# Performance work log

Measured on AMD Instinct MI355X. Metric: run time of the kernel, lower is better.

Reference implementation:

```python
import jax, jax.numpy as jnp
import numpy as np
import math

PAD_IDX = 1
BOS_IDX = 2
B, S, T = 32, 128, 64
E, H, L, V = 256, 512, 2, 32000


def _lstm_cell(gates, c):
    # torch gate order: i, f, g, o
    i, f, g, o = jnp.split(gates, 4, axis=-1)
    c_new = jax.nn.sigmoid(f) * c + jax.nn.sigmoid(i) * jnp.tanh(g)
    h_new = jax.nn.sigmoid(o) * jnp.tanh(c_new)
    return h_new, c_new


def _run_lstm_layer(x_tbi, Wih, Whh, b, h0, c0):
    def step(carry, x_t):
        h, c = carry
        h2, c2 = _lstm_cell(x_t @ Wih + h @ Whh + b, c)
        return (h2, c2), h2
    (hT, cT), ys = jax.lax.scan(step, (h0, c0), x_tbi)
    return ys, hT, cT


def setup_inputs() -> dict:
    key = jax.random.key(0)
    ks = iter(jax.random.split(key, 40))
    def w(shape, s=0.05):
        return jax.random.normal(next(ks), shape, jnp.float32) * s
    inp = {
        'src_tokens': jax.random.randint(next(ks), (B, S), 0, V, dtype=jnp.int32),
        'tgt_tokens': jax.random.randint(next(ks), (B, T), 0, V, dtype=jnp.int32),
        'src_emb': w((V, E), 0.02),
        'tgt_emb': w((V, E), 0.02),
        'enc_Wih0': w((E, 4 * H)), 'enc_Whh0': w((H, 4 * H)), 'enc_b0': jnp.zeros((4 * H,), jnp.float32),
        'enc_Wih1': w((H, 4 * H)), 'enc_Whh1': w((H, 4 * H)), 'enc_b1': jnp.zeros((4 * H,), jnp.float32),
        'dec_Wih0': w((E + H, 4 * H)), 'dec_Whh0': w((H, 4 * H)), 'dec_b0': jnp.zeros((4 * H,), jnp.float32),
        'dec_Wih1': w((H, 4 * H)), 'dec_Whh1': w((H, 4 * H)), 'dec_b1': jnp.zeros((4 * H,), jnp.float32),
        'attn_W': w((2 * H, H)), 'attn_b': jnp.zeros((H,), jnp.float32),
        'v_w': w((H,)),
        'coal_w': w((L, 1), 0.5), 'coal_b': jnp.zeros((1,), jnp.float32),
        'out_W': w((2 * H + E, V)), 'out_b': jnp.zeros((V,), jnp.float32),
    }
    return inp


def reference(src_tokens, tgt_tokens, src_emb, tgt_emb,
              enc_Wih0, enc_Whh0, enc_b0, enc_Wih1, enc_Whh1, enc_b1,
              dec_Wih0, dec_Whh0, dec_b0, dec_Wih1, dec_Whh1, dec_b1,
              attn_W, attn_b, v_w, coal_w, coal_b, out_W, out_b):
    Bq = src_tokens.shape[0]
    sqrtE_src = np.float32(math.sqrt(src_emb.shape[1]))
    sqrtE_tgt = np.float32(math.sqrt(tgt_emb.shape[1]))

    # ---- Encoder (2-layer LSTM, batch_first; dropout=0 eval) ----
    x = (src_emb[src_tokens] * sqrtE_src).transpose(1, 0, 2)  # (S,B,E)
    z = jnp.zeros((Bq, H), jnp.float32)
    ys0, hA, cA = _run_lstm_layer(x, enc_Wih0, enc_Whh0, enc_b0, z, z)
    ys1, hB, cB = _run_lstm_layer(ys0, enc_Wih1, enc_Whh1, enc_b1, z, z)
    enc_out = ys1.transpose(1, 0, 2)          # (B,S,H)
    hidden = jnp.stack([hA, hB])              # (L,B,H)
    cell = jnp.stack([cA, cB])

    mask = src_tokens != PAD_IDX              # (B,S)
    Wq, We = attn_W[:H], attn_W[H:]
    enc_proj = enc_out @ We                   # (B,S,H) loop-invariant part of attn linear

    def dec_step(carry, tok):
        h, c = carry                          # (L,B,H) each
        emb = jax.nn.relu(tgt_emb[tok] * sqrtE_tgt)          # (B,E)
        # faithful raw reshape (L,B,H) -> (B,H,L), coalesce layers
        q = jax.nn.relu(h.reshape(Bq, H, L) @ coal_w + coal_b)[..., 0]  # (B,H)
        e = jnp.tanh(enc_proj + (q @ Wq + attn_b)[:, None, :])          # (B,S,H)
        score = e @ v_w                                                 # (B,S)
        score = jnp.where(mask, score, np.float32(-1e10))
        a = jax.nn.softmax(score, axis=1)
        wctx = jnp.einsum('bs,bsh->bh', a, enc_out)                     # (B,H)
        xin = jnp.concatenate([emb, wctx], axis=-1)                     # (B,E+H)
        h0n, c0n = _lstm_cell(xin @ dec_Wih0 + h[0] @ dec_Whh0 + dec_b0, c[0])
        h1n, c1n = _lstm_cell(h0n @ dec_Wih1 + h[1] @ dec_Whh1 + dec_b1, c[1])
        logits = jnp.concatenate([h1n, wctx, emb], axis=-1) @ out_W + out_b  # (B,V)
        return (jnp.stack([h0n, h1n]), jnp.stack([c0n, c1n])), logits

    (hF, cF), outs = jax.lax.scan(dec_step, (hidden, cell), tgt_tokens[:, :-1].T)
    first = jnp.full((Bq, 1, out_b.shape[0]), np.float32(BOS_IDX))  # decoder_outputs[:,0]=BOS_IDX
    dec_outputs = jnp.concatenate([first, outs.transpose(1, 0, 2)], axis=1)  # (B,T,V)
    return dec_outputs, hF, cF
```

## Files before the change

kernel.cpp:

```cpp
#include <hip/hip_runtime.h>
#include <hip/hip_bf16.h>

typedef __bf16 bf16x8 __attribute__((ext_vector_type(8)));
typedef float f32x4 __attribute__((ext_vector_type(4)));
typedef unsigned long long u64;

#define DEV static __device__ __forceinline__

constexpr int Bq = 32, Sq = 128, Tq = 64, Eq = 256, Hq = 512, Vq = 32000;
constexpr int TD = 63;
constexpr int KOUT = 1280;
constexpr float SQRTE = 16.0f;

DEV float sigf(float x) { return 1.0f / (1.0f + __expf(-x)); }
DEV float tanh_fast(float x) {
    float ax = fabsf(x);
    float t = __expf(-2.f * ax);
    float r = (1.f - t) / (1.f + t);
    return x < 0.f ? -r : r;
}
DEV float tanh_c(float x) {
    float xc = fminf(fmaxf(x, -15.f), 15.f);
    float t = __expf(2.f * xc);
    return (t - 1.f) / (t + 1.f);
}

DEV u64 ldc(const u64* p) {
    return __hip_atomic_load(p, __ATOMIC_RELAXED, __HIP_MEMORY_SCOPE_AGENT);
}
DEV unsigned ldc32(const unsigned* p) {
    return __hip_atomic_load(p, __ATOMIC_RELAXED, __HIP_MEMORY_SCOPE_AGENT);
}
DEV void stc(u64* p, u64 v) {
    __hip_atomic_store(p, v, __ATOMIC_RELAXED, __HIP_MEMORY_SCOPE_AGENT);
}
DEV void stc32(unsigned* p, unsigned v) {
    __hip_atomic_store(p, v, __ATOMIC_RELAXED, __HIP_MEMORY_SCOPE_AGENT);
}
DEV unsigned short bfbits(float f) {
    __bf16 h = (__bf16)f;
    return __builtin_bit_cast(unsigned short, h);
}
DEV float bf2f(unsigned short u) {
    __bf16 h = __builtin_bit_cast(__bf16, u);
    return (float)h;
}
DEV u64 pack4bf(float a, float b, float c, float d) {
    return (u64)bfbits(a) | ((u64)bfbits(b) << 16) |
           ((u64)bfbits(c) << 32) | ((u64)bfbits(d) << 48);
}
DEV u64 pack2f(float a, float b) {
    return (u64)__float_as_uint(a) | ((u64)__float_as_uint(b) << 32);
}
template<bool C> DEV u64 ld64g(const u64* p) { return C ? ldc(p) : *p; }
template<bool C> DEV void st64g(u64* p, u64 v) { if (C) stc(p, v); else *p = v; }
DEV void drain_vm() { asm volatile("s_waitcnt vmcnt(0)" ::: "memory"); }

DEV void encwait(unsigned* flags, unsigned need0, unsigned need1) {
    __syncthreads();
    if (threadIdx.x < 64) {
        int lane = threadIdx.x;
        unsigned need = (lane < 32) ? need0 : need1;
        for (;;) {
            unsigned v = ldc32(flags + lane * 32);
            if (__all((int)(v >= need))) break;
            __builtin_amdgcn_s_sleep(1);
        }
    }
    __syncthreads();
}

__global__ __launch_bounds__(256) void k_embed_src(const int* __restrict__ tok,
                                                   const float* __restrict__ emb,
                                                   __hip_bfloat16* __restrict__ x)
{
    int idx = blockIdx.x * 256 + threadIdx.x;
    int e = idx & (Eq - 1);
    int r = idx >> 8;
    int b = r & 31, t = r >> 5;
    x[idx] = __float2bfloat16(emb[(size_t)tok[b * Sq + t] * Eq + e] * SQRTE);
}

__global__ __launch_bounds__(256) void k_embed_tgt(const int* __restrict__ tok,
                                                   const float* __restrict__ emb,
                                                   __hip_bfloat16* __restrict__ embt,
                                                   __hip_bfloat16* __restrict__ Xout)
{
    int idx = blockIdx.x * 256 + threadIdx.x;
    int e = idx & (Eq - 1);
    int r = idx >> 8;
    int b = r & 31, t = r >> 5;
    float v = fmaxf(0.f, emb[(size_t)tok[b * Tq + t] * Eq + e] * SQRTE);
    embt[idx] = __float2bfloat16(v);
    Xout[(size_t)r * KOUT + 1024 + e] = __float2bfloat16(v);
}

__global__ __launch_bounds__(256) void k_transpose_bf16(const float* __restrict__ W,
                                                        __hip_bfloat16* __restrict__ Wt,
                                                        int K, int N)
{
    __shared__ float tile[32][33];
    int nb = blockIdx.x * 32, kb = blockIdx.y * 32;
    int c = threadIdx.x & 31, r4 = threadIdx.x >> 5;
    for (int i = 0; i < 32; i += 8)
        tile[r4 + i][c] = W[(size_t)(kb + r4 + i) * N + nb + c];
    __syncthreads();
    for (int i = 0; i < 32; i += 8) {
        int rr = r4 + i;
        Wt[(size_t)(nb + rr) * K + kb + c] = __float2bfloat16(tile[c][rr]);
    }
}

struct TD10 {
    const float* s[10];
    __hip_bfloat16* d[10];
    int K[10];
    int N[10];
};
__global__ __launch_bounds__(256) void k_transpose_multi(TD10 td)
{
    __shared__ float tile[32][33];
    int m = blockIdx.y;
    int K = td.K[m], N = td.N[m];
    int ntn = N >> 5;
    int nb = (blockIdx.x % ntn) * 32;
    int kb = (blockIdx.x / ntn) * 32;
    if (kb >= K) return;
    const float* W = td.s[m];
    __hip_bfloat16* Wt = td.d[m];
    int c = threadIdx.x & 31, r4 = threadIdx.x >> 5;
    for (int i = 0; i < 32; i += 8)
        tile[r4 + i][c] = W[(size_t)(kb + r4 + i) * N + nb + c];
    __syncthreads();
    for (int i = 0; i < 32; i += 8) {
        int rr = r4 + i;
        Wt[(size_t)(nb + rr) * K + kb + c] = __float2bfloat16(tile[c][rr]);
    }
}

template<bool C>
DEV void stage_a(const u64* src, __bf16* As) {
    int tx = threadIdx.x;
#pragma unroll
    for (int p = 0; p < 8; ++p) {
        int c = tx + p * 256;
        int row = c >> 6, kc = c & 63;
        u64 v0 = ld64g<C>(src + c * 2);
        u64 v1 = ld64g<C>(src + c * 2 + 1);
        int kd = kc ^ (row & 7);
        *(u64*)(As + row * 512 + kd * 8) = v0;
        *(u64*)(As + row * 512 + kd * 8 + 4) = v1;
    }
}

DEV void mfma_pass(const __bf16* As, const unsigned short* BT, int colB,
                   int kg, int fr, f32x4* acc) {
    const unsigned short* bp = BT + (size_t)colB * 512 + kg * 8;
    int f7 = fr & 7;
#pragma unroll
    for (int k0 = 0; k0 < 512; k0 += 32) {
        int cidx = ((k0 >> 3) | kg) ^ f7;
        bf16x8 bfv = *(const bf16x8*)(bp + k0);
        bf16x8 af0 = *(const bf16x8*)(As + fr * 512 + cidx * 8);
        bf16x8 af1 = *(const bf16x8*)(As + (16 + fr) * 512 + cidx * 8);
        acc[0] = __builtin_amdgcn_mfma_f32_16x16x32_bf16(af0, bfv, acc[0], 0, 0, 0);
        acc[1] = __builtin_amdgcn_mfma_f32_16x16x32_bf16(af1, bfv, acc[1], 0, 0, 0);
    }
}

DEV void mfma_gates(const __bf16* As0, const __bf16* As1,
                    const __hip_bfloat16* B0T, const __hip_bfloat16* B1T,
                    int j0, float* gbuf)
{
    int tx = threadIdx.x, w = tx >> 6, lane = tx & 63;
    int fr = lane & 15, kg = lane >> 4;
    int colB = w * 512 + j0 + fr;
    f32x4 acc[2];
    acc[0] = (f32x4){0.f, 0.f, 0.f, 0.f};
    acc[1] = (f32x4){0.f, 0.f, 0.f, 0.f};
    mfma_pass(As0, (const unsigned short*)B0T, colB, kg, fr, acc);
    if (B1T) mfma_pass(As1, (const unsigned short*)B1T, colB, kg, fr, acc);
    __syncthreads();
    float* gw = gbuf + w * 512;
#pragma unroll
    for (int m = 0; m < 2; ++m)
#pragma unroll
        for (int qd = 0; qd < 4; ++qd)
            gw[(m * 16 + kg * 4 + qd) * 16 + fr] = acc[m][qd];
    __syncthreads();
}

template<bool C>
DEV void cell_epi(const float* gbuf,
                  const __hip_bfloat16* xpart, const float* bias,
                  float* cbuf, u64* hb, u64* hf,
                  __hip_bfloat16* eb, int ebs, int j0)
{
    int tx = threadIdx.x;
    if (tx >= 128) return;
    int b = tx >> 2, jg = tx & 3;
    int jj0 = jg * 4;
    int j = j0 + jj0;
    float g[4][4];
#pragma unroll
    for (int gi = 0; gi < 4; ++gi) {
        int idx = gi * 512 + b * 16 + jj0;
        float4 gv = *(const float4*)(gbuf + idx);
        g[gi][0] = gv.x; g[gi][1] = gv.y; g[gi][2] = gv.z; g[gi][3] = gv.w;
        if (xpart) {
            u64 xv = *(const u64*)((const unsigned short*)xpart + b * 2048 + gi * 512 + j);
#pragma unroll
            for (int e = 0; e < 4; ++e)
                g[gi][e] += bf2f((unsigned short)(xv >> (16 * e)));
        }
        if (bias) {
            float4 bv = *(const float4*)(bias + gi * 512 + j);
            g[gi][0] += bv.x; g[gi][1] += bv.y; g[gi][2] += bv.z; g[gi][3] += bv.w;
        }
    }
    float4 cv = *(float4*)(cbuf + b * 512 + j);
    float cc[4] = {cv.x, cv.y, cv.z, cv.w};
    float hv[4];
#pragma unroll
    for (int e = 0; e < 4; ++e) {
        float cn = sigf(g[1][e]) * cc[e] + sigf(g[0][e]) * tanh_fast(g[2][e]);
        cc[e] = cn;
        hv[e] = sigf(g[3][e]) * tanh_fast(cn);
    }
    *(float4*)(cbuf + b * 512 + j) = make_float4(cc[0], cc[1], cc[2], cc[3]);
    u64 hpk = pack4bf(hv[0], hv[1], hv[2], hv[3]);
    st64g<C>(hb + ((b * 512 + j) >> 2), hpk);
    st64g<C>(hf + ((b * 512 + j) >> 1), pack2f(hv[0], hv[1]));
    st64g<C>(hf + ((b * 512 + j) >> 1) + 1, pack2f(hv[2], hv[3]));
    if (eb) st64g<C>((u64*)(eb + (size_t)b * ebs + j), hpk);
}

__global__ __launch_bounds__(256) void k_enc_persist(
    const __hip_bfloat16* __restrict__ X0b,
    const __hip_bfloat16* __restrict__ eWhh0T, const __hip_bfloat16* __restrict__ eWih1T,
    const __hip_bfloat16* __restrict__ eWhh1T, const float* __restrict__ eb1,
    __hip_bfloat16* __restrict__ h0b, __hip_bfloat16* __restrict__ h1b,
    float* __restrict__ h0f, float* __restrict__ h1f,
    float* __restrict__ c0, float* __restrict__ c1,
    __hip_bfloat16* __restrict__ ys0b,
    __hip_bfloat16* __restrict__ encb,
    unsigned* __restrict__ flags)
{
    __shared__ __align__(16) char shm[65536];
    __bf16* As0 = (__bf16*)shm;
    __bf16* As1 = (__bf16*)(shm + 32768);
    bool lay1 = blockIdx.x >= 32;
    int j0 = (blockIdx.x & 31) * 16;

    if (!lay1) {
        for (int t = 0; t < 128; ++t) {
            encwait(flags, (unsigned)t, 0u);
            stage_a<true>((const u64*)(h0b + (t & 1) * 16384), As0);
            __syncthreads();
            mfma_gates(As0, nullptr, eWhh0T, nullptr, j0, (float*)As0);
            cell_epi<true>((float*)As0, X0b + (size_t)t * 32 * 2048, nullptr,
                           c0, (u64*)(h0b + ((t + 1) & 1) * 16384), (u64*)h0f,
                           ys0b + (size_t)t * 16384, 512, j0);
            __syncthreads();
            if (threadIdx.x == 0) {
                drain_vm();
                stc32(flags + blockIdx.x * 32, (unsigned)(t + 1));
            }
        }
    } else {
        for (int s = 0; s < 128; ++s) {
            encwait(flags, (unsigned)(s + 1), (unsigned)s);
            stage_a<true>((const u64*)(ys0b + (size_t)s * 16384), As0);
            stage_a<true>((const u64*)(h1b + (s & 1) * 16384), As1);
            __syncthreads();
            mfma_gates(As0, As1, eWih1T, eWhh1T, j0, (float*)As0);
            cell_epi<true>((float*)As0, nullptr, eb1,
                           c1, (u64*)(h1b + ((s + 1) & 1) * 16384), (u64*)h1f,
                           encb + s * 512, 128 * 512, j0);
            __syncthreads();
            if (threadIdx.x == 0) {
                drain_vm();
                stc32(flags + blockIdx.x * 32, (unsigned)(s + 1));
            }
        }
    }
}

__global__ __launch_bounds__(256) void k_dattn2(
    const __hip_bfloat16* __restrict__ enc_projb, const __hip_bfloat16* __restrict__ enc_outb,
    const int* __restrict__ src_tok, const float* __restrict__ v_w,
    const float* __restrict__ attn_W, const float* __restrict__ attn_b,
    const float* __restrict__ coal_w, const float* __restrict__ coal_b,
    const float* __restrict__ h0fc, const float* __restrict__ h1fc,
    __hip_bfloat16* __restrict__ wctxb, __hip_bfloat16* __restrict__ XoutT)
{
    __shared__ float q[512];
    __shared__ float aqs[512];
    __shared__ float vws[512];
    __shared__ float ws[128];
    __shared__ float rinvs;
    int b = blockIdx.x, tx = threadIdx.x;

    const float* hrow = (b < 16) ? (h0fc + b * 1024) : (h1fc + (b - 16) * 1024);
    float cw0 = coal_w[0], cw1 = coal_w[1], cb = coal_b[0];
    for (int j = tx; j < 512; j += 256) {
        float2 pv = *(const float2*)(hrow + 2 * j);
        q[j] = fmaxf(0.f, pv.x * cw0 + pv.y * cw1 + cb);
    }
    for (int i = tx; i < 512; i += 256) vws[i] = v_w[i];
    __syncthreads();
    float a0 = attn_b[tx], a1 = attn_b[tx + 256];
#pragma unroll 8
    for (int j = 0; j < 512; ++j) {
        float qj = q[j];
        a0 += qj * attn_W[(size_t)j * 512 + tx];
        a1 += qj * attn_W[(size_t)j * 512 + tx + 256];
    }
    aqs[tx] = a0; aqs[tx + 256] = a1;
    __syncthreads();
    int s = tx >> 1, half = tx & 1;
    const unsigned short* epr = (const unsigned short*)enc_projb
                                + ((size_t)(b * 128 + s)) * 512 + half * 256;
    float s0 = 0.f, s1 = 0.f, s2 = 0.f, s3 = 0.f;
#pragma unroll 4
    for (int ii = 0; ii < 256; ii += 8) {
        bf16x8 f8 = *(const bf16x8*)(epr + ii);
        int ib = half * 256 + ii;
        s0 += tanh_c((float)f8[0] + aqs[ib])     * vws[ib];
        s1 += tanh_c((float)f8[1] + aqs[ib + 1]) * vws[ib + 1];
        s2 += tanh_c((float)f8[2] + aqs[ib + 2]) * vws[ib + 2];
        s3 += tanh_c((float)f8[3] + aqs[ib + 3]) * vws[ib + 3];
        s0 += tanh_c((float)f8[4] + aqs[ib + 4]) * vws[ib + 4];
        s1 += tanh_c((float)f8[5] + aqs[ib + 5]) * vws[ib + 5];
        s2 += tanh_c((float)f8[6] + aqs[ib + 6]) * vws[ib + 6];
        s3 += tanh_c((float)f8[7] + aqs[ib + 7]) * vws[ib + 7];
    }
    float p = (s0 + s1) + (s2 + s3);
    p += __shfl_xor(p, 1, 64);
    if (half == 0)
        ws[s] = (src_tok[b * 128 + s] != 1) ? __expf(p) : 0.f;
    __syncthreads();
    if (tx < 64) {
        float ss = ws[tx] + ws[tx + 64];
#pragma unroll
        for (int o = 32; o > 0; o >>= 1) ss += __shfl_down(ss, o, 64);
        if (tx == 0) rinvs = 1.0f / ss;
    }
    __syncthreads();
    float rinv = rinvs;
    const unsigned short* eo = (const unsigned short*)enc_outb + (size_t)b * 65536;
    int i0 = tx * 2;
    float c0a = 0.f, c1a = 0.f;
#pragma unroll 4
    for (int s2i = 0; s2i < 128; ++s2i) {
        unsigned pk2 = *(const unsigned*)(eo + (size_t)s2i * 512 + i0);
        float wv = ws[s2i];
        c0a += wv * bf2f((unsigned short)(pk2 & 0xffffu));
        c1a += wv * bf2f((unsigned short)(pk2 >> 16));
    }
    c0a *= rinv; c1a *= rinv;
    unsigned pk = (unsigned)bfbits(c0a) | ((unsigned)bfbits(c1a) << 16);
    *((unsigned*)wctxb + ((b * 512 + i0) >> 1)) = pk;
    *((unsigned*)XoutT + (((size_t)b * KOUT + 512 + i0) >> 1)) = pk;
}

__global__ __launch_bounds__(256) void k_rec(
    const __hip_bfloat16* __restrict__ A0, const __hip_bfloat16* __restrict__ B0T,
    const __hip_bfloat16* __restrict__ A1, const __hip_bfloat16* __restrict__ B1T,
    const __hip_bfloat16* __restrict__ xpart, const float* __restrict__ bias,
    float* __restrict__ cbuf, float* __restrict__ hf, __hip_bfloat16* __restrict__ hb,
    __hip_bfloat16* __restrict__ ebf16, int ebs)
{
    __shared__ __align__(16) char shm[65536];
    __bf16* As0 = (__bf16*)shm;
    __bf16* As1 = (__bf16*)(shm + 32768);
    int j0 = blockIdx.x * 16;
    stage_a<false>((const u64*)A0, As0);
    stage_a<false>((const u64*)A1, As1);
    __syncthreads();
    mfma_gates(As0, As1, B0T, B1T, j0, (float*)As0);
    cell_epi<false>((float*)As0, xpart, bias, cbuf, (u64*)hb, (u64*)hf, ebf16, ebs, j0);
}

__global__ __launch_bounds__(256) void k_mfma(
    const __hip_bfloat16* __restrict__ A, const __hip_bfloat16* __restrict__ BT,
    const float* __restrict__ bias, float* __restrict__ Cf,
    __hip_bfloat16* __restrict__ Cb, int M, int N, int K)
{
    __shared__ __bf16 As[128][72];
    __shared__ __bf16 Bs[128][72];
    const unsigned short* Aw = (const unsigned short*)A;
    const unsigned short* Bw = (const unsigned short*)BT;
    int n0 = blockIdx.x * 128, m0 = blockIdx.y * 128;
    int tx = threadIdx.x;
    int w = tx >> 6, lane = tx & 63;
    int wm = (w >> 1) * 64, wn = (w & 1) * 64;
    int fr = lane & 15, kg = lane >> 4;
    f32x4 acc[4][4];
#pragma unroll
    for (int mi = 0; mi < 4; mi++)
#pragma unroll
        for (int ni = 0; ni < 4; ni++) acc[mi][ni] = (f32x4){0.f, 0.f, 0.f, 0.f};

    for (int k0 = 0; k0 < K; k0 += 64) {
        __syncthreads();
#pragma unroll
        for (int p = 0; p < 4; p++) {
            int ch = tx + p * 256;
            int r = ch >> 3, cc = (ch & 7) * 8;
            uint4 va = {0u, 0u, 0u, 0u};
            int m = m0 + r;
            if (m < M) va = *(const uint4*)(Aw + (size_t)m * K + k0 + cc);
            *(uint4*)(&As[r][cc]) = va;
            uint4 vb = *(const uint4*)(Bw + (size_t)(n0 + r) * K + k0 + cc);
            *(uint4*)(&Bs[r][cc]) = vb;
        }
        __syncthreads();
#pragma unroll
        for (int kk = 0; kk < 64; kk += 32) {
            bf16x8 af[4], bfv[4];
#pragma unroll
            for (int i = 0; i < 4; i++) {
                af[i]  = *(const bf16x8*)(&As[wm + i * 16 + fr][kk + kg * 8]);
                bfv[i] = *(const bf16x8*)(&Bs[wn + i * 16 + fr][kk + kg * 8]);
            }
#pragma unroll
            for (int mi = 0; mi < 4; mi++)
#pragma unroll
                for (int ni = 0; ni < 4; ni++)
                    acc[mi][ni] = __builtin_amdgcn_mfma_f32_16x16x32_bf16(
                        af[mi], bfv[ni], acc[mi][ni], 0, 0, 0);
        }
    }
#pragma unroll
    for (int ni = 0; ni < 4; ni++) {
        int n = n0 + wn + ni * 16 + fr;
        float bv = bias ? bias[n] : 0.f;
#pragma unroll
        for (int mi = 0; mi < 4; mi++) {
#pragma unroll
            for (int qd = 0; qd < 4; qd++) {
                int R = m0 + wm + mi * 16 + kg * 4 + qd;
                if (R < M) {
                    float v = acc[mi][ni][qd] + bv;
                    if (Cf) Cf[(size_t)R * N + n] = v;
                    else    Cb[(size_t)R * N + n] = __float2bfloat16(v);
                }
            }
        }
    }
}

__global__ __launch_bounds__(256) void k_init_dec(
    const float* __restrict__ h0e, const float* __restrict__ h1e,
    const float* __restrict__ c0e, const float* __restrict__ c1e,
    float* __restrict__ h0fd, float* __restrict__ h1fd,
    __hip_bfloat16* __restrict__ h0bd, __hip_bfloat16* __restrict__ h1bd,
    float* __restrict__ c0d, float* __restrict__ c1d)
{
    int idx = blockIdx.x * 256 + threadIdx.x;
    float a = h0e[idx], b = h1e[idx];
    h0fd[idx] = a; h1fd[idx] = b;
    h0bd[idx] = __float2bfloat16(a);
    h1bd[idx] = __float2bfloat16(b);
    c0d[idx] = c0e[idx];
    c1d[idx] = c1e[idx];
}

__global__ __launch_bounds__(256) void k_bos(float* __restrict__ out)
{
    int b = blockIdx.y;
    int i = blockIdx.x * 256 + threadIdx.x;
    out[(size_t)b * (Tq * Vq) + i] = 2.0f;
}

__global__ __launch_bounds__(256) void k_finalize(
    const float* __restrict__ h0f, const float* __restrict__ h1f,
    const float* __restrict__ c0f, const float* __restrict__ c1f,
    float* __restrict__ out)
{
    int idx = blockIdx.x * 256 + threadIdx.x;
    size_t base = (size_t)Bq * Tq * Vq;
    out[base + idx] = h0f[idx];
    out[base + 16384 + idx] = h1f[idx];
    out[base + 32768 + idx] = c0f[idx];
    out[base + 49152 + idx] = c1f[idx];
}

__global__ __launch_bounds__(256) void k_logits(
    const __hip_bfloat16* __restrict__ A, const __hip_bfloat16* __restrict__ Bt,
    const float* __restrict__ bias, float* __restrict__ out)
{
    __shared__ __bf16 As[128][72];
    __shared__ __bf16 Bs[128][72];
    const unsigned short* Aw = (const unsigned short*)A;
    const unsigned short* Bw = (const unsigned short*)Bt;
    int n0 = blockIdx.x * 128, m0 = blockIdx.y * 128;
    int tx = threadIdx.x;
    int w = tx >> 6, lane = tx & 63;
    int wm = (w >> 1) * 64, wn = (w & 1) * 64;
    int fr = lane & 15, kg = lane >> 4;
    f32x4 acc[4][4];
#pragma unroll
    for (int mi = 0; mi < 4; mi++)
#pragma unroll
        for (int ni = 0; ni < 4; ni++) acc[mi][ni] = (f32x4){0.f, 0.f, 0.f, 0.f};

    for (int k0 = 0; k0 < 1280; k0 += 64) {
        __syncthreads();
#pragma unroll
        for (int p = 0; p < 4; p++) {
            int ch = tx + p * 256;
            int r = ch >> 3, cc = (ch & 7) * 8;
            uint4 va = {0u, 0u, 0u, 0u};
            int m = m0 + r;
            if (m < 2016) va = *(const uint4*)(Aw + (size_t)m * 1280 + k0 + cc);
            *(uint4*)(&As[r][cc]) = va;
            uint4 vb = *(const uint4*)(Bw + (size_t)(n0 + r) * 1280 + k0 + cc);
            *(uint4*)(&Bs[r][cc]) = vb;
        }
        __syncthreads();
#pragma unroll
        for (int kk = 0; kk < 64; kk += 32) {
            bf16x8 af[4], bfv[4];
#pragma unroll
            for (int i = 0; i < 4; i++) {
                af[i]  = *(const bf16x8*)(&As[wm + i * 16 + fr][kk + kg * 8]);
                bfv[i] = *(const bf16x8*)(&Bs[wn + i * 16 + fr][kk + kg * 8]);
            }
#pragma unroll
            for (int mi = 0; mi < 4; mi++)
#pragma unroll
                for (int ni = 0; ni < 4; ni++)
                    acc[mi][ni] = __builtin_amdgcn_mfma_f32_16x16x32_bf16(
                        af[mi], bfv[ni], acc[mi][ni], 0, 0, 0);
        }
    }
#pragma unroll
    for (int ni = 0; ni < 4; ni++) {
        int n = n0 + wn + ni * 16 + fr;
        float bv = bias[n];
#pragma unroll
        for (int mi = 0; mi < 4; mi++) {
#pragma unroll
            for (int qd = 0; qd < 4; qd++) {
                int R = m0 + wm + mi * 16 + kg * 4 + qd;
                if (R < 2016) {
                    int bb = R & 31, ts = R >> 5;
                    out[(size_t)bb * (Tq * Vq) + (size_t)(ts + 1) * Vq + n] =
                        acc[mi][ni][qd] + bv;
                }
            }
        }
    }
}

extern "C" void kernel_launch(void* const* d_in, const int* in_sizes, int n_in,
                              void* d_out, int out_size, void* d_ws, size_t ws_size,
                              hipStream_t stream)
{
    (void)in_sizes; (void)n_in; (void)out_size; (void)ws_size;
    const int*   src_tok = (const int*)  d_in[0];
    const int*   tgt_tok = (const int*)  d_in[1];
    const float* src_emb = (const float*)d_in[2];
    const float* tgt_emb = (const float*)d_in[3];
    const float* eWih0   = (const float*)d_in[4];
    const float* eWhh0   = (const float*)d_in[5];
    const float* eb0     = (const float*)d_in[6];
    const float* eWih1   = (const float*)d_in[7];
    const float* eWhh1   = (const float*)d_in[8];
    const float* eb1     = (const float*)d_in[9];
    const float* dWih0   = (const float*)d_in[10];
    const float* dWhh0   = (const float*)d_in[11];
    const float* db0     = (const float*)d_in[12];
    const float* dWih1   = (const float*)d_in[13];
    const float* dWhh1   = (const float*)d_in[14];
    const float* db1     = (const float*)d_in[15];
    const float* attn_W  = (const float*)d_in[16];
    const float* attn_b  = (const float*)d_in[17];
    const float* v_w     = (const float*)d_in[18];
    const float* coal_w  = (const float*)d_in[19];
    const float* coal_b  = (const float*)d_in[20];
    const float* out_W   = (const float*)d_in[21];
    const float* out_b   = (const float*)d_in[22];
    float* out = (float*)d_out;

    char* ws = (char*)d_ws;
    size_t off = 0;
    auto alloc = [&](size_t bytes) -> char* {
        char* p = ws + off;
        off += (bytes + 255) & ~(size_t)255;
        return p;
    };
    typedef __hip_bfloat16 BF;
    BF* X0b     = (BF*)alloc(4096ull * 2048 * 2);
    BF* Xembb   = (BF*)alloc(2016ull * 2048 * 2);
    BF* x_srcb  = (BF*)alloc(4096ull * 256 * 2);
    BF* embtb   = (BF*)alloc(2016ull * 256 * 2);
    BF* ys0b    = (BF*)alloc(128ull * 16384 * 2);
    BF* enc_outb  = (BF*)alloc(4096ull * 512 * 2);
    BF* enc_projb = (BF*)alloc(4096ull * 512 * 2);
    BF* wctxb     = (BF*)alloc(16384ull * 2);
    BF* Xout      = (BF*)alloc(2016ull * 1280 * 2);
    BF* Wt        = (BF*)alloc(32000ull * 1280 * 2);
    BF* eWhh0T  = (BF*)alloc(2048ull * 512 * 2);
    BF* eWih1T  = (BF*)alloc(2048ull * 512 * 2);
    BF* eWhh1T  = (BF*)alloc(2048ull * 512 * 2);
    BF* dWih0wT = (BF*)alloc(2048ull * 512 * 2);
    BF* dWhh0T  = (BF*)alloc(2048ull * 512 * 2);
    BF* dWih1T  = (BF*)alloc(2048ull * 512 * 2);
    BF* dWhh1T  = (BF*)alloc(2048ull * 512 * 2);
    BF* eWih0T  = (BF*)alloc(2048ull * 256 * 2);
    BF* dWih0eT = (BF*)alloc(2048ull * 256 * 2);
    BF* WeT     = (BF*)alloc(512ull * 512 * 2);
    BF* h0b_e   = (BF*)alloc(2ull * 16384 * 2);
    BF* h1b_e   = (BF*)alloc(2ull * 16384 * 2);
    float* h0f_e = (float*)alloc(16384ull * 4);
    float* h1f_e = (float*)alloc(16384ull * 4);
    float* c0e   = (float*)alloc(16384ull * 4);
    float* c1e   = (float*)alloc(16384ull * 4);
    float* h0fd  = (float*)alloc(2ull * 16384 * 4);
    float* h1fd  = (float*)alloc(2ull * 16384 * 4);
    BF* h0bd     = (BF*)alloc(2ull * 16384 * 2);
    BF* h1bd     = (BF*)alloc(2ull * 16384 * 2);
    float* c0d   = (float*)alloc(16384ull * 4);
    float* c1d   = (float*)alloc(16384ull * 4);
    unsigned* encFlags = (unsigned*)alloc(64 * 32 * 4);

    hipMemsetAsync(encFlags, 0, 64 * 32 * 4, stream);
    hipMemsetAsync(h0b_e, 0, 2 * 16384 * 2, stream);
    hipMemsetAsync(h1b_e, 0, 2 * 16384 * 2, stream);
    hipMemsetAsync(c0e, 0, 16384 * 4, stream);
    hipMemsetAsync(c1e, 0, 16384 * 4, stream);

    k_embed_src<<<4096, 256, 0, stream>>>(src_tok, src_emb, x_srcb);
    k_embed_tgt<<<2016, 256, 0, stream>>>(tgt_tok, tgt_emb, embtb, Xout);

    TD10 td;
    td.s[0] = eWhh0;              td.d[0] = eWhh0T;  td.K[0] = 512; td.N[0] = 2048;
    td.s[1] = eWih1;              td.d[1] = eWih1T;  td.K[1] = 512; td.N[1] = 2048;
    td.s[2] = eWhh1;              td.d[2] = eWhh1T;  td.K[2] = 512; td.N[2] = 2048;
    td.s[3] = dWih0 + 256 * 2048; td.d[3] = dWih0wT; td.K[3] = 512; td.N[3] = 2048;
    td.s[4] = dWhh0;              td.d[4] = dWhh0T;  td.K[4] = 512; td.N[4] = 2048;
    td.s[5] = dWih1;              td.d[5] = dWih1T;  td.K[5] = 512; td.N[5] = 2048;
    td.s[6] = dWhh1;              td.d[6] = dWhh1T;  td.K[6] = 512; td.N[6] = 2048;
    td.s[7] = eWih0;              td.d[7] = eWih0T;  td.K[7] = 256; td.N[7] = 2048;
    td.s[8] = dWih0;              td.d[8] = dWih0eT; td.K[8] = 256; td.N[8] = 2048;
    td.s[9] = attn_W + 512 * 512; td.d[9] = WeT;     td.K[9] = 512; td.N[9] = 512;
    k_transpose_multi<<<dim3(1024, 10), 256, 0, stream>>>(td);
    k_transpose_bf16<<<dim3(1000, 40), 256, 0, stream>>>(out_W, Wt, 1280, 32000);

    k_mfma<<<dim3(16, 32), 256, 0, stream>>>(x_srcb, eWih0T, eb0, nullptr, X0b, 4096, 2048, 256);
    k_mfma<<<dim3(16, 16), 256, 0, stream>>>(embtb, dWih0eT, db0, nullptr, Xembb, 2016, 2048, 256);
    k_bos<<<dim3(125, 32), 256, 0, stream>>>(out);

    k_enc_persist<<<64, 256, 0, stream>>>(X0b, eWhh0T, eWih1T, eWhh1T, eb1,
                                          h0b_e, h1b_e, h0f_e, h1f_e, c0e, c1e,
                                          ys0b, enc_outb, encFlags);

    k_mfma<<<dim3(4, 32), 256, 0, stream>>>(enc_outb, WeT, nullptr, nullptr, enc_projb, 4096, 512, 512);

    k_init_dec<<<64, 256, 0, stream>>>(h0f_e, h1f_e, c0e, c1e,
                                       h0fd, h1fd, h0bd, h1bd, c0d, c1d);

    for (int t = 0; t < TD; ++t) {
        int cur = t & 1, nxt = cur ^ 1;
        BF* XoutT = Xout + (size_t)t * 32 * KOUT;
        k_dattn2<<<32, 256, 0, stream>>>(enc_projb, enc_outb, src_tok, v_w,
                                         attn_W, attn_b, coal_w, coal_b,
                                         h0fd + cur * 16384, h1fd + cur * 16384,
                                         wctxb, XoutT);
        k_rec<<<32, 256, 0, stream>>>(wctxb, dWih0wT,
                                      h0bd + cur * 16384, dWhh0T,
                                      Xembb + (size_t)t * 32 * 2048, nullptr,
                                      c0d, h0fd + nxt * 16384, h0bd + nxt * 16384,
                                      nullptr, 0);
        k_rec<<<32, 256, 0, stream>>>(h0bd + nxt * 16384, dWih1T,
                                      h1bd + cur * 16384, dWhh1T,
                                      nullptr, db1,
                                      c1d, h1fd + nxt * 16384, h1bd + nxt * 16384,
                                      XoutT, KOUT);
    }

    k_finalize<<<64, 256, 0, stream>>>(h0fd + (TD & 1) * 16384, h1fd + (TD & 1) * 16384,
                                       c0d, c1d, out);
    k_logits<<<dim3(250, 16), 256, 0, stream>>>(Xout, Wt, out_b, out);
}
```

Before: 5.297 ms.

## Fuse decoder LSTM layers into one kernel and overlap per-step logits GEMM

Replaces the two per-step k_rec launches with a single k_dcells launch. In it, 32 blocks compute layer 0, 32 blocks spin on flags before computing layer 1, and 250 extra blocks compute the previous step's output-projection logits. The final k_logits launch then only handles the last step's rows. The aim is to remove one launch per step and to hide the large logits GEMM inside the latency-bound recurrence. The cost is a spin-wait between co-resident blocks, which can deadlock if the layer-1 blocks are scheduled before layer 0, and a logits GEMM with no LDS reuse that reads its operands straight from global memory.

Result: slower. 6.057 ms (+14.3%).

```diff
diff --git a/kernel.cpp b/kernel.cpp
--- a/kernel.cpp
+++ b/kernel.cpp
@@ -361,25 +361,98 @@
     c0a *= rinv; c1a *= rinv;
     unsigned pk = (unsigned)bfbits(c0a) | ((unsigned)bfbits(c1a) << 16);
     *((unsigned*)wctxb + ((b * 512 + i0) >> 1)) = pk;
-    *((unsigned*)XoutT + (((size_t)b * KOUT + 512 + i0) >> 1)) = pk;
-}
-
-__global__ __launch_bounds__(256) void k_rec(
-    const __hip_bfloat16* __restrict__ A0, const __hip_bfloat16* __restrict__ B0T,
-    const __hip_bfloat16* __restrict__ A1, const __hip_bfloat16* __restrict__ B1T,
-    const __hip_bfloat16* __restrict__ xpart, const float* __restrict__ bias,
-    float* __restrict__ cbuf, float* __restrict__ hf, __hip_bfloat16* __restrict__ hb,
-    __hip_bfloat16* __restrict__ ebf16, int ebs)
+    *((unsigned*)XoutT + (((size_t)b * KOUT + i0 + 512) >> 1)) = pk;
+}
+
+__global__ __launch_bounds__(256) void k_dcells(
+    const __hip_bfloat16* __restrict__ wctxb,
+    const __hip_bfloat16* __restrict__ Wih0wT, const __hip_bfloat16* __restrict__ Whh0T,
+    const __hip_bfloat16* __restrict__ Wih1T, const __hip_bfloat16* __restrict__ Whh1T,
+    const float* __restrict__ db1, const __hip_bfloat16* __restrict__ xpart,
+    const __hip_bfloat16* __restrict__ h0b_cur, __hip_bfloat16* __restrict__ h0b_nxt,
+    float* __restrict__ h0f_nxt,
+    const __hip_bfloat16* __restrict__ h1b_cur, __hip_bfloat16* __restrict__ h1b_nxt,
+    float* __restrict__ h1f_nxt,
+    float* __restrict__ c0d, float* __restrict__ c1d,
+    __hip_bfloat16* __restrict__ XoutT,
+    unsigned* __restrict__ flags, unsigned ep,
+    const __hip_bfloat16* __restrict__ Xout_prev, const __hip_bfloat16* __restrict__ Wt,
+    const float* __restrict__ out_b, float* __restrict__ out, int tprev)
 {
     __shared__ __align__(16) char shm[65536];
     __bf16* As0 = (__bf16*)shm;
     __bf16* As1 = (__bf16*)(shm + 32768);
-    int j0 = blockIdx.x * 16;
-    stage_a<false>((const u64*)A0, As0);
-    stage_a<false>((const u64*)A1, As1);
-    __syncthreads();
-    mfma_gates(As0, As1, B0T, B1T, j0, (float*)As0);
-    cell_epi<false>((float*)As0, xpart, bias, cbuf, (u64*)hb, (u64*)hf, ebf16, ebs, j0);
+    int bid = blockIdx.x, tx = threadIdx.x;
+
+    if (bid < 32) {
+        int j0 = bid * 16;
+        stage_a<false>((const u64*)wctxb, As0);
+        stage_a<false>((const u64*)h0b_cur, As1);
+        __syncthreads();
+        mfma_gates(As0, As1, Wih0wT, Whh0T, j0, (float*)As0);
+        cell_epi<true>((float*)As0, xpart, nullptr,
+                       c0d, (u64*)h0b_nxt, (u64*)h0f_nxt, nullptr, 0, j0);
+        __syncthreads();
+        if (tx == 0) {
+            drain_vm();
+            stc32(flags + bid * 32, ep);
+        }
+    } else if (bid < 64) {
+        int j0 = (bid - 32) * 16;
+        stage_a<false>((const u64*)h1b_cur, As1);
+        __syncthreads();
+        if (tx < 64) {
+            int lane = tx;
+            for (;;) {
+                unsigned v = (lane < 32) ? ldc32(flags + lane * 32) : ep;
+                if (__all((int)(v >= ep))) break;
+                __builtin_amdgcn_s_sleep(1);
+            }
+        }
+        __syncthreads();
+        stage_a<true>((const u64*)h0b_nxt, As0);
+        __syncthreads();
+        mfma_gates(As0, As1, Wih1T, Whh1T, j0, (float*)As0);
+        cell_epi<false>((float*)As0, nullptr, db1,
+                        c1d, (u64*)h1b_nxt, (u64*)h1f_nxt, XoutT, KOUT, j0);
+    } else {
+        if (tprev < 0) return;
+        int n0 = (bid - 64) * 128;
+        const unsigned short* At = (const unsigned short*)Xout_prev;
+        const unsigned short* Wtu = (const unsigned short*)Wt;
+        int w = tx >> 6, lane = tx & 63, fr = lane & 15, kg = lane >> 4;
+        int nbase = n0 + w * 32;
+        f32x4 acc[2][2];
+        acc[0][0] = (f32x4){0.f, 0.f, 0.f, 0.f};
+        acc[0][1] = (f32x4){0.f, 0.f, 0.f, 0.f};
+        acc[1][0] = (f32x4){0.f, 0.f, 0.f, 0.f};
+        acc[1][1] = (f32x4){0.f, 0.f, 0.f, 0.f};
+#pragma unroll 4
+        for (int kk = 0; kk < 1280; kk += 32) {
+            bf16x8 a0 = *(const bf16x8*)(At + (size_t)fr * KOUT + kk + kg * 8);
+            bf16x8 a1 = *(const bf16x8*)(At + (size_t)(16 + fr) * KOUT + kk + kg * 8);
+            bf16x8 b0 = *(const bf16x8*)(Wtu + (size_t)(nbase + fr) * 1280 + kk + kg * 8);
+            bf16x8 b1 = *(const bf16x8*)(Wtu + (size_t)(nbase + 16 + fr) * 1280 + kk + kg * 8);
+            acc[0][0] = __builtin_amdgcn_mfma_f32_16x16x32_bf16(a0, b0, acc[0][0], 0, 0, 0);
+            acc[0][1] = __builtin_amdgcn_mfma_f32_16x16x32_bf16(a0, b1, acc[0][1], 0, 0, 0);
+            acc[1][0] = __builtin_amdgcn_mfma_f32_16x16x32_bf16(a1, b0, acc[1][0], 0, 0, 0);
+            acc[1][1] = __builtin_amdgcn_mfma_f32_16x16x32_bf16(a1, b1, acc[1][1], 0, 0, 0);
+        }
+#pragma unroll
+        for (int ni = 0; ni < 2; ++ni) {
+            int n = nbase + ni * 16 + fr;
+            float bv = out_b[n];
+#pragma unroll
+            for (int mi = 0; mi < 2; ++mi) {
+#pragma unroll
+                for (int qd = 0; qd < 4; ++qd) {
+                    int b = mi * 16 + kg * 4 + qd;
+                    out[(size_t)b * (Tq * Vq) + (size_t)(tprev + 1) * Vq + n] =
+                        acc[mi][ni][qd] + bv;
+                }
+            }
+        }
+    }
 }
 
 __global__ __launch_bounds__(256) void k_mfma(
@@ -489,13 +562,13 @@
 
 __global__ __launch_bounds__(256) void k_logits(
     const __hip_bfloat16* __restrict__ A, const __hip_bfloat16* __restrict__ Bt,
-    const float* __restrict__ bias, float* __restrict__ out)
+    const float* __restrict__ bias, float* __restrict__ out, int m_off)
 {
     __shared__ __bf16 As[128][72];
     __shared__ __bf16 Bs[128][72];
     const unsigned short* Aw = (const unsigned short*)A;
     const unsigned short* Bw = (const unsigned short*)Bt;
-    int n0 = blockIdx.x * 128, m0 = blockIdx.y * 128;
+    int n0 = blockIdx.x * 128, m0 = blockIdx.y * 128 + m_off;
     int tx = threadIdx.x;
     int w = tx >> 6, lane = tx & 63;
     int wm = (w >> 1) * 64, wn = (w & 1) * 64;
@@ -626,8 +699,10 @@
     float* c0d   = (float*)alloc(16384ull * 4);
     float* c1d   = (float*)alloc(16384ull * 4);
     unsigned* encFlags = (unsigned*)alloc(64 * 32 * 4);
+    unsigned* decFlags = (unsigned*)alloc(32 * 32 * 4);
 
     hipMemsetAsync(encFlags, 0, 64 * 32 * 4, stream);
+    hipMemsetAsync(decFlags, 0, 32 * 32 * 4, stream);
     hipMemsetAsync(h0b_e, 0, 2 * 16384 * 2, stream);
     hipMemsetAsync(h1b_e, 0, 2 * 16384 * 2, stream);
     hipMemsetAsync(c0e, 0, 16384 * 4, stream);
@@ -666,23 +741,23 @@
     for (int t = 0; t < TD; ++t) {
         int cur = t & 1, nxt = cur ^ 1;
         BF* XoutT = Xout + (size_t)t * 32 * KOUT;
+        const BF* XoutPrev = Xout + (size_t)(t > 0 ? t - 1 : 0) * 32 * KOUT;
         k_dattn2<<<32, 256, 0, stream>>>(enc_projb, enc_outb, src_tok, v_w,
                                          attn_W, attn_b, coal_w, coal_b,
                                          h0fd + cur * 16384, h1fd + cur * 16384,
                                          wctxb, XoutT);
-        k_rec<<<32, 256, 0, stream>>>(wctxb, dWih0wT,
-                                      h0bd + cur * 16384, dWhh0T,
-                                      Xembb + (size_t)t * 32 * 2048, nullptr,
-                                      c0d, h0fd + nxt * 16384, h0bd + nxt * 16384,
-                                      nullptr, 0);
-        k_rec<<<32, 256, 0, stream>>>(h0bd + nxt * 16384, dWih1T,
-                                      h1bd + cur * 16384, dWhh1T,
-                                      nullptr, db1,
-                                      c1d, h1fd + nxt * 16384, h1bd + nxt * 16384,
-                                      XoutT, KOUT);
+        k_dcells<<<314, 256, 0, stream>>>(wctxb, dWih0wT, dWhh0T, dWih1T, dWhh1T, db1,
+                                          Xembb + (size_t)t * 32 * 2048,
+                                          h0bd + cur * 16384, h0bd + nxt * 16384,
+                                          h0fd + nxt * 16384,
+                                          h1bd + cur * 16384, h1bd + nxt * 16384,
+                                          h1fd + nxt * 16384,
+                                          c0d, c1d, XoutT,
+                                          decFlags, (unsigned)(t + 1),
+                                          XoutPrev, Wt, out_b, out, t - 1);
     }
 
     k_finalize<<<64, 256, 0, stream>>>(h0fd + (TD & 1) * 16384, h1fd + (TD & 1) * 16384,
                                        c0d, c1d, out);
-    k_logits<<<dim3(250, 16), 256, 0, stream>>>(Xout, Wt, out_b, out);
-}
+    k_logits<<<dim3(250, 1), 256, 0, stream>>>(Xout, Wt, out_b, out, 1920);
+}
```
